# Performance work log

Measured on AMD Instinct MI355X. Metric: run time of the kernel, lower is better.

The kernel has to match this reference:

```python
import jax, jax.numpy as jnp
import numpy as np

B, S, D, H, L, V, DFF = 2, 2048, 1024, 16, 4, 32000, 4096
DH = D // H
STD = 0.02
EPS = 1e-5


def _sinusoidal_pe(seq_len, d_model):
    pos = np.arange(seq_len)[:, None].astype(np.float32)
    div = np.exp(np.arange(0, d_model, 2).astype(np.float32) * (-np.log(10000.0) / d_model))
    pe = np.zeros((seq_len, d_model), dtype=np.float32)
    pe[:, 0::2] = np.sin(pos * div)
    pe[:, 1::2] = np.cos(pos * div)
    return jnp.asarray(pe)


def _layernorm(x, g, b):
    mu = jnp.mean(x, axis=-1, keepdims=True)
    var = jnp.mean(jnp.square(x - mu), axis=-1, keepdims=True)
    return (x - mu) * jax.lax.rsqrt(var + EPS) * g + b


def setup_inputs() -> dict:
    key = jax.random.key(0)
    ks = jax.random.split(key, 12)
    input_ids = jax.random.randint(ks[0], (B, S), 0, V)
    tok_emb = STD * jax.random.normal(ks[1], (V, D), dtype=jnp.float32)
    tok_emb = tok_emb.at[0].set(0.0)  # padding_idx=0 zeroed
    Wq = STD * jax.random.normal(ks[2], (L, D, D), dtype=jnp.float32)
    Wk = STD * jax.random.normal(ks[3], (L, D, D), dtype=jnp.float32)
    Wv = STD * jax.random.normal(ks[4], (L, D, D), dtype=jnp.float32)
    Wo = STD * jax.random.normal(ks[5], (L, D, D), dtype=jnp.float32)
    W1 = STD * jax.random.normal(ks[6], (L, D, DFF), dtype=jnp.float32)
    W2 = STD * jax.random.normal(ks[7], (L, DFF, D), dtype=jnp.float32)
    Wout = STD * jax.random.normal(ks[8], (D, V), dtype=jnp.float32)
    zD = jnp.zeros((L, D), dtype=jnp.float32)
    return {
        'input_ids': input_ids, 'tok_emb': tok_emb,
        'Wq': Wq, 'bq': zD, 'Wk': Wk, 'bk': zD, 'Wv': Wv, 'bv': zD, 'Wo': Wo, 'bo': zD,
        'ln1_g': jnp.ones((L, D), jnp.float32), 'ln1_b': zD,
        'W1': W1, 'b1': jnp.zeros((L, DFF), jnp.float32), 'W2': W2, 'b2': zD,
        'ln3_g': jnp.ones((L, D), jnp.float32), 'ln3_b': zD,
        'Wout': Wout, 'bout': jnp.zeros((V,), jnp.float32),
    }


def reference(input_ids, tok_emb, Wq, bq, Wk, bk, Wv, bv, Wo, bo,
              ln1_g, ln1_b, W1, b1, W2, b2, ln3_g, ln3_b, Wout, bout):
    pe = _sinusoidal_pe(S, D)
    causal = jnp.tril(jnp.ones((S, S), dtype=bool))  # [S,S]
    x = tok_emb[input_ids] * jnp.float32(np.sqrt(D)) + pe  # [B,S,D]
    scale = jnp.float32(1.0 / np.sqrt(DH))
    for l in range(L):
        q = (x @ Wq[l] + bq[l]).reshape(B, S, H, DH).transpose(0, 2, 1, 3)
        k = (x @ Wk[l] + bk[l]).reshape(B, S, H, DH).transpose(0, 2, 1, 3)
        v = (x @ Wv[l] + bv[l]).reshape(B, S, H, DH).transpose(0, 2, 1, 3)
        scores = jnp.einsum('bhqd,bhkd->bhqk', q, k) * scale
        scores = jnp.where(causal, scores, jnp.float32(-1e9))
        attn = jax.nn.softmax(scores, axis=-1)
        o = jnp.einsum('bhqk,bhkd->bhqd', attn, v)
        o = o.transpose(0, 2, 1, 3).reshape(B, S, D) @ Wo[l] + bo[l]
        x = _layernorm(x + o, ln1_g[l], ln1_b[l])
        f = jax.nn.relu(x @ W1[l] + b1[l]) @ W2[l] + b2[l]
        x = _layernorm(x + f, ln3_g[l], ln3_b[l])
    logits = x @ Wout + bout  # [B,S,V]
    return logits
```

## Files before the change

kernel.cpp:

```cpp
#include <hip/hip_runtime.h>
#include <stdint.h>

typedef unsigned short u16;
typedef __attribute__((ext_vector_type(8))) short bf16x8;
typedef __attribute__((ext_vector_type(4))) float f32x4;

#define NB 2
#define NS 2048
#define ND 1024
#define NH 16
#define NL 4
#define NV 32000
#define NF 4096
#define NDH 64
#define NM (NB*NS)

__device__ __forceinline__ u16 f2b(float f) {
  union { float f; uint32_t u; } v; v.f = f;
  uint32_t r = v.u + 0x7FFFu + ((v.u >> 16) & 1u);
  return (u16)(r >> 16);
}

#define GLOAD_LDS16(gp, lp) __builtin_amdgcn_global_load_lds( \
    (const __attribute__((address_space(1))) void*)(gp), \
    (__attribute__((address_space(3))) void*)(lp), 16, 0, 0)

#define VMCNT8 do { asm volatile("s_waitcnt vmcnt(8)" ::: "memory"); __builtin_amdgcn_sched_barrier(0); } while (0)
#define VMCNT0 do { asm volatile("s_waitcnt vmcnt(0)" ::: "memory"); __builtin_amdgcn_sched_barrier(0); } while (0)
#define LGKM0  do { asm volatile("s_waitcnt lgkmcnt(0)" ::: "memory"); __builtin_amdgcn_sched_barrier(0); } while (0)
#define MFMA16(a,b,c) __builtin_amdgcn_mfma_f32_16x16x32_bf16((a),(b),(c),0,0,0)

__global__ __launch_bounds__(256)
void k_transpose64(const float* __restrict__ w, u16* __restrict__ wt, int K, int N) {
  __shared__ float tile[64][65];
  const int n0 = blockIdx.x * 64;
  const int k0 = blockIdx.y * 64;
  const int tr = threadIdx.x >> 4;
  const int tc = (threadIdx.x & 15) * 4;
#pragma unroll
  for (int i = 0; i < 4; i++) {
    int r = tr + i * 16;
    float4 v = *(const float4*)(w + (size_t)(k0 + r) * N + n0 + tc);
    tile[r][tc + 0] = v.x; tile[r][tc + 1] = v.y;
    tile[r][tc + 2] = v.z; tile[r][tc + 3] = v.w;
  }
  __syncthreads();
#pragma unroll
  for (int i = 0; i < 4; i++) {
    int nn = tr + i * 16;
    ushort4 pk;
    pk.x = f2b(tile[tc + 0][nn]);
    pk.y = f2b(tile[tc + 1][nn]);
    pk.z = f2b(tile[tc + 2][nn]);
    pk.w = f2b(tile[tc + 3][nn]);
    *(ushort4*)(wt + (size_t)(n0 + nn) * K + k0 + tc) = pk;
  }
}

__global__ __launch_bounds__(256)
void k_embed(const int* __restrict__ ids, const float* __restrict__ emb,
             float* __restrict__ x, u16* __restrict__ xb) {
  int row = blockIdx.x;
  int s = row & (NS - 1);
  int tok = ids[row];
  const float* e = emb + (size_t)tok * ND;
  int d0 = threadIdx.x * 4;
  float y[4];
#pragma unroll
  for (int j = 0; j < 4; j++) {
    int dd = d0 + j;
    float di = (float)(dd & ~1);
    float dv = expf(di * (-9.210340371976184f / (float)ND));
    float ang = (float)s * dv;
    float pe = (dd & 1) ? cosf(ang) : sinf(ang);
    y[j] = e[dd] * 32.0f + pe;
  }
  float4 w; w.x = y[0]; w.y = y[1]; w.z = y[2]; w.w = y[3];
  *(float4*)(x + (size_t)row * ND + d0) = w;
  uint2 pk;
  pk.x = (uint32_t)f2b(y[0]) | ((uint32_t)f2b(y[1]) << 16);
  pk.y = (uint32_t)f2b(y[2]) | ((uint32_t)f2b(y[3]) << 16);
  *(uint2*)(xb + (size_t)row * ND + d0) = pk;
}

__global__ __launch_bounds__(256)
void k_ln(const float* __restrict__ xin, const float* __restrict__ add,
          const float* __restrict__ g, const float* __restrict__ bb,
          float* __restrict__ xout, u16* __restrict__ xbout) {
  int row = blockIdx.x;
  int t = threadIdx.x;
  const float4 xi = *(const float4*)(xin + (size_t)row * ND + t * 4);
  const float4 ai = *(const float4*)(add + (size_t)row * ND + t * 4);
  float v0 = xi.x + ai.x, v1 = xi.y + ai.y, v2 = xi.z + ai.z, v3 = xi.w + ai.w;
  float s = v0 + v1 + v2 + v3;
  float s2 = v0 * v0 + v1 * v1 + v2 * v2 + v3 * v3;
#pragma unroll
  for (int d = 32; d >= 1; d >>= 1) { s += __shfl_xor(s, d); s2 += __shfl_xor(s2, d); }
  __shared__ float rs[8];
  int w = t >> 6;
  if ((t & 63) == 0) { rs[w] = s; rs[4 + w] = s2; }
  __syncthreads();
  s = rs[0] + rs[1] + rs[2] + rs[3];
  s2 = rs[4] + rs[5] + rs[6] + rs[7];
  float mu = s * (1.0f / ND);
  float var = s2 * (1.0f / ND) - mu * mu;
  float rr = rsqrtf(var + 1e-5f);
  const float4 gg = *(const float4*)(g + t * 4);
  const float4 be = *(const float4*)(bb + t * 4);
  float y0 = (v0 - mu) * rr * gg.x + be.x;
  float y1 = (v1 - mu) * rr * gg.y + be.y;
  float y2 = (v2 - mu) * rr * gg.z + be.z;
  float y3 = (v3 - mu) * rr * gg.w + be.w;
  float4 yo; yo.x = y0; yo.y = y1; yo.z = y2; yo.w = y3;
  *(float4*)(xout + (size_t)row * ND + t * 4) = yo;
  uint2 pk;
  pk.x = (uint32_t)f2b(y0) | ((uint32_t)f2b(y1) << 16);
  pk.y = (uint32_t)f2b(y2) | ((uint32_t)f2b(y3) << 16);
  *(uint2*)(xbout + (size_t)row * ND + t * 4) = pk;
}

template<int MODE>
__global__ __launch_bounds__(256)
void k_gemm_bt(const u16* __restrict__ A, const u16* __restrict__ Bt,
               const float* __restrict__ bias0, const float* __restrict__ bias1,
               const float* __restrict__ bias2,
               float* __restrict__ Cf, u16* __restrict__ Cb,
               int M, int N, int K, float scale) {
  constexpr int BM = 128, BN = 128, BK = 32;
  __shared__ __align__(16) u16 As[2][BM * BK];
  __shared__ __align__(16) u16 Bs[2][BN * BK];

  const int tid = threadIdx.x;
  const int lane = tid & 63;
  const int wave = tid >> 6;

  const int bm = blockIdx.x * BM;
  const int bn = blockIdx.y * BN;

  const int wr = (wave >> 1) * 64;
  const int wc = (wave & 1) * 64;
  const int lr = lane & 15;
  const int lk = (lane >> 4) * 8;

  const u16* Abase = A + (size_t)bm * K;
  const u16* Bbase = Bt + (size_t)bn * K;
  const int srow = lane >> 2;
  const int scol = (lane & 3) * 8;

  auto stage = [&](int buf, int kt) {
    const u16* Ag = Abase + (size_t)kt * BK + scol;
    const u16* Bg = Bbase + (size_t)kt * BK + scol;
#pragma unroll
    for (int i = 0; i < 2; i++) {
      const int rbase = (i * 4 + wave) * 16;
      GLOAD_LDS16(Ag + (size_t)(rbase + srow) * K, &As[buf][rbase * BK]);
      GLOAD_LDS16(Bg + (size_t)(rbase + srow) * K, &Bs[buf][rbase * BK]);
    }
  };

  f32x4 acc[4][4] = {};
  const int nk = K / BK;
  stage(0, 0);
  for (int kt = 0; kt < nk; ++kt) {
    __syncthreads();
    if (kt + 1 < nk) stage((kt + 1) & 1, kt + 1);
    const int buf = kt & 1;
    bf16x8 af[4], bfv[4];
#pragma unroll
    for (int m = 0; m < 4; m++)
      af[m] = *(const bf16x8*)(&As[buf][(wr + m * 16 + lr) * BK + lk]);
#pragma unroll
    for (int n = 0; n < 4; n++)
      bfv[n] = *(const bf16x8*)(&Bs[buf][(wc + n * 16 + lr) * BK + lk]);
#pragma unroll
    for (int m = 0; m < 4; m++)
#pragma unroll
      for (int n = 0; n < 4; n++)
        acc[m][n] = MFMA16(af[m], bfv[n], acc[m][n]);
  }

  const int lg = lane >> 4;
#pragma unroll
  for (int m = 0; m < 4; m++) {
#pragma unroll
    for (int n = 0; n < 4; n++) {
      int col = bn + wc + n * 16 + lr;
      float bv;
      if (MODE == 3) {
        int which = col >> 10;
        int cc = col & 1023;
        const float* bp = (which == 0) ? bias0 : ((which == 1) ? bias1 : bias2);
        bv = bp[cc];
      } else {
        bv = bias0[col];
      }
      if (MODE == 3 && (col >> 10) == 2) {
        int cc = col & 1023;
        int row0 = bm + wr + m * 16 + lg * 4;
        int b_ = row0 >> 11;
        int s_ = row0 & (NS - 1);
        int h_ = cc >> 6;
        int dh = cc & 63;
        ushort4 pk;
        pk.x = f2b(acc[m][n][0] + bv);
        pk.y = f2b(acc[m][n][1] + bv);
        pk.z = f2b(acc[m][n][2] + bv);
        pk.w = f2b(acc[m][n][3] + bv);
        *(ushort4*)(Cb + (size_t)2 * NM * ND +
                    ((((size_t)b_ * NH + h_) * NDH) + dh) * NS + s_) = pk;
        continue;
      }
#pragma unroll
      for (int j = 0; j < 4; j++) {
        int row = bm + wr + m * 16 + lg * 4 + j;
        float v = acc[m][n][j] + bv;
        if (MODE == 0) {
          Cf[(size_t)row * N + col] = v;
        } else if (MODE == 1) {
          Cb[(size_t)row * N + col] = f2b(fmaxf(v, 0.0f));
        } else {
          int which = col >> 10;
          int cc = col & 1023;
          if (which == 0) v *= scale;
          int b_ = row >> 11;
          int s_ = row & (NS - 1);
          int h_ = cc >> 6;
          int dh = cc & 63;
          Cb[(size_t)which * ((size_t)NM * ND) +
             ((((size_t)b_ * NH + h_) * NS) + s_) * NDH + dh] = f2b(v);
        }
      }
    }
  }
}

__global__ __launch_bounds__(256)
void k_gemm64(const u16* __restrict__ A, const u16* __restrict__ Bt,
              const float* __restrict__ bias,
              float* __restrict__ Cf, int M, int N, int K) {
  constexpr int BM = 64, BN = 128, BK = 32;
  __shared__ __align__(16) u16 As[2][BM * BK];
  __shared__ __align__(16) u16 Bs[2][BN * BK];

  const int tid = threadIdx.x;
  const int lane = tid & 63;
  const int wave = tid >> 6;

  const int bm = blockIdx.x * BM;
  const int bn = blockIdx.y * BN;

  const int wr = (wave >> 1) * 32;
  const int wc = (wave & 1) * 64;
  const int lr = lane & 15;
  const int lk = (lane >> 4) * 8;

  const u16* Abase = A + (size_t)bm * K;
  const u16* Bbase = Bt + (size_t)bn * K;
  const int srow = lane >> 2;
  const int scol = (lane & 3) * 8;

  auto stage = [&](int buf, int kt) {
    const u16* Ag = Abase + (size_t)kt * BK + scol;
    const u16* Bg = Bbase + (size_t)kt * BK + scol;
#pragma unroll
    for (int i = 0; i < 3; i++) {
      const int c = i * 4 + wave;
      if (c < 4) {
        const int rbase = c * 16;
        GLOAD_LDS16(Ag + (size_t)(rbase + srow) * K, &As[buf][rbase * BK]);
      } else {
        const int rbase = (c - 4) * 16;
        GLOAD_LDS16(Bg + (size_t)(rbase + srow) * K, &Bs[buf][rbase * BK]);
      }
    }
  };

  f32x4 acc[2][4] = {};
  const int nk = K / BK;
  stage(0, 0);
  for (int kt = 0; kt < nk; ++kt) {
    __syncthreads();
    if (kt + 1 < nk) stage((kt + 1) & 1, kt + 1);
    const int buf = kt & 1;
    bf16x8 af[2], bfv[4];
#pragma unroll
    for (int m = 0; m < 2; m++)
      af[m] = *(const bf16x8*)(&As[buf][(wr + m * 16 + lr) * BK + lk]);
#pragma unroll
    for (int n = 0; n < 4; n++)
      bfv[n] = *(const bf16x8*)(&Bs[buf][(wc + n * 16 + lr) * BK + lk]);
#pragma unroll
    for (int m = 0; m < 2; m++)
#pragma unroll
      for (int n = 0; n < 4; n++)
        acc[m][n] = MFMA16(af[m], bfv[n], acc[m][n]);
  }

  const int lg = lane >> 4;
#pragma unroll
  for (int m = 0; m < 2; m++) {
#pragma unroll
    for (int n = 0; n < 4; n++) {
      int col = bn + wc + n * 16 + lr;
      float bv = bias[col];
#pragma unroll
      for (int j = 0; j < 4; j++) {
        int row = bm + wr + m * 16 + lg * 4 + j;
        Cf[(size_t)row * N + col] = acc[m][n][j] + bv;
      }
    }
  }
}

template<int MODE>
__global__ __launch_bounds__(512, 2)
void k_gemm256(const u16* __restrict__ A, const u16* __restrict__ Bt,
               const float* __restrict__ bias,
               float* __restrict__ Cf, u16* __restrict__ Cb,
               int M, int N, int K) {
  __shared__ __align__(16) u16 As2[2][256 * 64];
  __shared__ __align__(16) u16 Bs2[2][256 * 64];

  const int tid = threadIdx.x;
  const int lane = tid & 63;
  const int wave = tid >> 6;
  const int wrM = wave >> 2;
  const int wcN = wave & 3;
  const int lr = lane & 15;
  const int g = lane >> 4;
  const int r7 = lr & 7;

  const int bm = blockIdx.x * 256;
  const int bn = blockIdx.y * 256;

  const int srow_in = lane >> 3;
  const int schunk = lane & 7;
  const int sq = (schunk ^ srow_in) * 8;

  auto stageA = [&](int buf, int t) {
#pragma unroll
    for (int s2 = 0; s2 < 4; ++s2) {
      const int rbase = (s2 * 8 + wave) * 8;
      GLOAD_LDS16(A + (size_t)(bm + rbase + srow_in) * K + t * 64 + sq, &As2[buf][rbase * 64]);
    }
  };
  auto stageB = [&](int buf, int t) {
#pragma unroll
    for (int s2 = 0; s2 < 4; ++s2) {
      const int rbase = (s2 * 8 + wave) * 8;
      GLOAD_LDS16(Bt + (size_t)(bn + rbase + srow_in) * K + t * 64 + sq, &Bs2[buf][rbase * 64]);
    }
  };

  f32x4 acc[8][4] = {};
  const int NT = K / 64;

  stageA(0, 0); stageB(0, 0);
  stageA(1, 1); stageB(1, 1);

  for (int t = 0; t < NT; ++t) {
    const int buf = t & 1;
    if (t + 1 < NT) { VMCNT8; } else { VMCNT0; }
    __builtin_amdgcn_s_barrier();

    const char* ab = (const char*)(&As2[buf][0]);
    const char* bb2 = (const char*)(&Bs2[buf][0]);
    bf16x8 aF[4][2], bF[4][2];

#pragma unroll
    for (int m = 0; m < 4; m++) {
      int row = wrM * 128 + m * 16 + lr;
      aF[m][0] = *(const bf16x8*)(ab + row * 128 + ((g ^ r7) * 16));
      aF[m][1] = *(const bf16x8*)(ab + row * 128 + (((4 + g) ^ r7) * 16));
    }
#pragma unroll
    for (int n = 0; n < 2; n++) {
      int row = wcN * 64 + n * 16 + lr;
      bF[n][0] = *(const bf16x8*)(bb2 + row * 128 + ((g ^ r7) * 16));
      bF[n][1] = *(const bf16x8*)(bb2 + row * 128 + (((4 + g) ^ r7) * 16));
    }
    __builtin_amdgcn_s_barrier();
    LGKM0;
    __builtin_amdgcn_s_setprio(1);
#pragma unroll
    for (int m = 0; m < 4; m++)
#pragma unroll
      for (int n = 0; n < 2; n++) {
        acc[m][n] = MFMA16(aF[m][0], bF[n][0], acc[m][n]);
        acc[m][n] = MFMA16(aF[m][1], bF[n][1], acc[m][n]);
      }
    __builtin_amdgcn_s_setprio(0);
    __builtin_amdgcn_s_barrier();

#pragma unroll
    for (int n = 2; n < 4; n++) {
      int row = wcN * 64 + n * 16 + lr;
      bF[n][0] = *(const bf16x8*)(bb2 + row * 128 + ((g ^ r7) * 16));
      bF[n][1] = *(const bf16x8*)(bb2 + row * 128 + (((4 + g) ^ r7) * 16));
    }
    __builtin_amdgcn_s_barrier();
    LGKM0;
    __builtin_amdgcn_s_setprio(1);
#pragma unroll
    for (int m = 0; m < 4; m++)
#pragma unroll
      for (int n = 2; n < 4; n++) {
        acc[m][n] = MFMA16(aF[m][0], bF[n][0], acc[m][n]);
        acc[m][n] = MFMA16(aF[m][1], bF[n][1], acc[m][n]);
      }
    __builtin_amdgcn_s_setprio(0);
    __builtin_amdgcn_s_barrier();

#pragma unroll
    for (int m = 0; m < 4; m++) {
      int row = wrM * 128 + (m + 4) * 16 + lr;
      aF[m][0] = *(const bf16x8*)(ab + row * 128 + ((g ^ r7) * 16));
      aF[m][1] = *(const bf16x8*)(ab + row * 128 + (((4 + g) ^ r7) * 16));
    }
    if (t + 2 < NT) stageB(buf, t + 2);
    __builtin_amdgcn_s_barrier();
    LGKM0;
    __builtin_amdgcn_s_setprio(1);
#pragma unroll
    for (int m = 0; m < 4; m++)
#pragma unroll
      for (int n = 0; n < 2; n++) {
        acc[m + 4][n] = MFMA16(aF[m][0], bF[n][0], acc[m + 4][n]);
        acc[m + 4][n] = MFMA16(aF[m][1], bF[n][1], acc[m + 4][n]);
      }
    __builtin_amdgcn_s_setprio(0);
    __builtin_amdgcn_s_barrier();

    if (t + 2 < NT) stageA(buf, t + 2);
    __builtin_amdgcn_s_barrier();
    __builtin_amdgcn_s_setprio(1);
#pragma unroll
    for (int m = 0; m < 4; m++)
#pragma unroll
      for (int n = 2; n < 4; n++) {
        acc[m + 4][n] = MFMA16(aF[m][0], bF[n][0], acc[m + 4][n]);
        acc[m + 4][n] = MFMA16(aF[m][1], bF[n][1], acc[m + 4][n]);
      }
    __builtin_amdgcn_s_setprio(0);
    __builtin_amdgcn_s_barrier();
  }

#pragma unroll
  for (int m = 0; m < 8; m++) {
#pragma unroll
    for (int n = 0; n < 4; n++) {
      int col = bn + wcN * 64 + n * 16 + lr;
      float bv = bias[col];
#pragma unroll
      for (int j = 0; j < 4; j++) {
        int row = bm + wrM * 128 + m * 16 + g * 4 + j;
        float v = acc[m][n][j] + bv;
        if (MODE == 0) Cf[(size_t)row * N + col] = v;
        else           Cb[(size_t)row * N + col] = f2b(fmaxf(v, 0.0f));
      }
    }
  }
}

__global__ __launch_bounds__(256)
void k_attn(const u16* __restrict__ Q, const u16* __restrict__ Kq,
            const u16* __restrict__ Vt, u16* __restrict__ O) {
  const int qt = blockIdx.x;
  const int bh = blockIdx.y;
  const int b_ = bh >> 4, h_ = bh & 15;
  const int tid = threadIdx.x, lane = tid & 63, wave = tid >> 6;
  const int lr = lane & 15, lg = lane >> 4;

  __shared__ __align__(16) u16 Ks[64 * 64];
  __shared__ __align__(16) u16 Vs[64 * 64];
  __shared__ __align__(16) u16 Ps[4][16 * 64];

  const size_t base = (size_t)bh * NS * NDH;
  bf16x8 qf0, qf1;
  {
    const u16* qp = Q + base + (size_t)(qt * 64 + wave * 16 + lr) * NDH;
    qf0 = *(const bf16x8*)(qp + lg * 8);
    qf1 = *(const bf16x8*)(qp + 32 + lg * 8);
  }

  const int idx0 = tid, idx1 = tid + 256;
  const int r0 = idx0 >> 3, r1 = idx1 >> 3;
  const int c0 = (idx0 & 7) * 8, c1 = (idx1 & 7) * 8;
  const int so0 = r0 * 128 + ((c0 * 2) ^ ((r0 & 7) << 4));
  const int so1 = r1 * 128 + ((c1 * 2) ^ ((r1 & 7) << 4));

  bf16x8 rk0, rk1, rv0, rv1;
  auto loadregs = [&](int kt2) {
    const u16* Kg = Kq + base + (size_t)(kt2 * 64) * NDH;
    const u16* Vg = Vt + base + kt2 * 64;
    rk0 = *(const bf16x8*)(Kg + (size_t)r0 * NDH + c0);
    rk1 = *(const bf16x8*)(Kg + (size_t)r1 * NDH + c1);
    rv0 = *(const bf16x8*)(Vg + (size_t)r0 * NS + c0);
    rv1 = *(const bf16x8*)(Vg + (size_t)r1 * NS + c1);
  };

  float mrun[4] = {-1e30f, -1e30f, -1e30f, -1e30f};
  float lrun[4] = {0.f, 0.f, 0.f, 0.f};
  f32x4 oacc[4] = {};
  const int q0 = qt * 64 + wave * 16;

  loadregs(0);
  for (int kt2 = 0; kt2 <= qt; ++kt2) {
    *(bf16x8*)((char*)Ks + so0) = rk0;
    *(bf16x8*)((char*)Ks + so1) = rk1;
    *(bf16x8*)((char*)Vs + so0) = rv0;
    *(bf16x8*)((char*)Vs + so1) = rv1;
    __syncthreads();
    if (kt2 < qt) loadregs(kt2 + 1);

    f32x4 sc[4];
    __builtin_amdgcn_s_setprio(1);
#pragma unroll
    for (int c = 0; c < 4; c++) {
      int row = c * 16 + lr;
      const char* kp = (const char*)Ks + row * 128;
      int sm = (row & 7) << 4;
      bf16x8 k0 = *(const bf16x8*)(kp + ((lg * 16) ^ sm));
      bf16x8 k1 = *(const bf16x8*)(kp + ((64 + lg * 16) ^ sm));
      f32x4 s = {};
      s = MFMA16(qf0, k0, s);
      s = MFMA16(qf1, k1, s);
      sc[c] = s;
    }
    __builtin_amdgcn_s_setprio(0);

    if (kt2 == qt) {
#pragma unroll
      for (int c = 0; c < 4; c++)
#pragma unroll
        for (int j = 0; j < 4; j++) {
          int qg = q0 + lg * 4 + j;
          int kg = qt * 64 + c * 16 + lr;
          if (kg > qg) sc[c][j] = -1e9f;
        }
    }

#pragma unroll
    for (int j = 0; j < 4; j++) {
      float mt = fmaxf(fmaxf(sc[0][j], sc[1][j]), fmaxf(sc[2][j], sc[3][j]));
#pragma unroll
      for (int d = 8; d >= 1; d >>= 1) mt = fmaxf(mt, __shfl_xor(mt, d));
      float mnew = fmaxf(mrun[j], mt);
      float corr = __expf(mrun[j] - mnew);
      float ps = 0.f;
#pragma unroll
      for (int c = 0; c < 4; c++) {
        float p = __expf(sc[c][j] - mnew);
        sc[c][j] = p;
        ps += p;
      }
#pragma unroll
      for (int d = 8; d >= 1; d >>= 1) ps += __shfl_xor(ps, d);
      lrun[j] = lrun[j] * corr + ps;
      mrun[j] = mnew;
#pragma unroll
      for (int n = 0; n < 4; n++) oacc[n][j] *= corr;
    }

    char* pw = (char*)Ps[wave];
#pragma unroll
    for (int c = 0; c < 4; c++)
#pragma unroll
      for (int j = 0; j < 4; j++) {
        int row = lg * 4 + j;
        *(u16*)(pw + row * 128 + ((((c * 16 + lr) * 2)) ^ ((row & 7) << 4))) = f2b(sc[c][j]);
      }

    {
      int smq = (lr & 7) << 4;
      bf16x8 pa0 = *(const bf16x8*)(pw + lr * 128 + ((lg * 16) ^ smq));
      bf16x8 pa1 = *(const bf16x8*)(pw + lr * 128 + ((64 + lg * 16) ^ smq));
      __builtin_amdgcn_s_setprio(1);
#pragma unroll
      for (int n = 0; n < 4; n++) {
        int row = n * 16 + lr;
        const char* vp = (const char*)Vs + row * 128;
        int sm = (row & 7) << 4;
        bf16x8 v0 = *(const bf16x8*)(vp + ((lg * 16) ^ sm));
        bf16x8 v1 = *(const bf16x8*)(vp + ((64 + lg * 16) ^ sm));
        oacc[n] = MFMA16(pa0, v0, oacc[n]);
        oacc[n] = MFMA16(pa1, v1, oacc[n]);
      }
      __builtin_amdgcn_s_setprio(0);
    }
    __syncthreads();
  }

#pragma unroll
  for (int j = 0; j < 4; j++) {
    float inv = 1.0f / lrun[j];
    int s_ = qt * 64 + wave * 16 + lg * 4 + j;
    size_t orow = ((size_t)b_ * NS + s_) * ND + h_ * NDH;
#pragma unroll
    for (int n = 0; n < 4; n++)
      O[orow + n * 16 + lr] = f2b(oacc[n][j] * inv);
  }
}

extern "C" void kernel_launch(void* const* d_in, const int* in_sizes, int n_in,
                              void* d_out, int out_size, void* d_ws, size_t ws_size,
                              hipStream_t stream) {
  const int* ids = (const int*)d_in[0];
  const float* tok_emb = (const float*)d_in[1];
  const float* Wq = (const float*)d_in[2];
  const float* bq = (const float*)d_in[3];
  const float* Wk = (const float*)d_in[4];
  const float* bk = (const float*)d_in[5];
  const float* Wv = (const float*)d_in[6];
  const float* bv = (const float*)d_in[7];
  const float* Wo = (const float*)d_in[8];
  const float* bo = (const float*)d_in[9];
  const float* ln1g = (const float*)d_in[10];
  const float* ln1b = (const float*)d_in[11];
  const float* W1 = (const float*)d_in[12];
  const float* b1 = (const float*)d_in[13];
  const float* W2 = (const float*)d_in[14];
  const float* b2 = (const float*)d_in[15];
  const float* ln3g = (const float*)d_in[16];
  const float* ln3b = (const float*)d_in[17];
  const float* Wout = (const float*)d_in[18];
  const float* bout = (const float*)d_in[19];
  float* out = (float*)d_out;

  char* ws = (char*)d_ws;
  size_t off = 0;
  auto alloc = [&](size_t bytes) -> void* {
    void* p = ws + off;
    off += (bytes + 255) & ~(size_t)255;
    return p;
  };
  float* x    = (float*)alloc((size_t)NM * ND * 4);
  float* tmp  = (float*)alloc((size_t)NM * ND * 4);
  u16* xb     = (u16*)alloc((size_t)NM * ND * 2);
  u16* hb     = (u16*)alloc((size_t)NM * NF * 2);
  u16* qkvb   = (u16*)alloc((size_t)3 * NM * ND * 2);
  u16* ob     = (u16*)alloc((size_t)NM * ND * 2);
  u16* Wqkvt  = (u16*)alloc((size_t)NL * 3 * ND * ND * 2);
  u16* Wot    = (u16*)alloc((size_t)NL * ND * ND * 2);
  u16* W1t    = (u16*)alloc((size_t)NL * (size_t)NF * ND * 2);
  u16* W2t    = (u16*)alloc((size_t)NL * (size_t)ND * NF * 2);
  u16* Woutt  = (u16*)alloc((size_t)NV * ND * 2);

  for (int l = 0; l < NL; l++) {
    size_t wl = (size_t)l * ND * ND;
    u16* qkvl = Wqkvt + (size_t)l * 3 * ND * ND;
    dim3 gdd(ND / 64, ND / 64);
    k_transpose64<<<gdd, 256, 0, stream>>>(Wq + wl, qkvl, ND, ND);
    k_transpose64<<<gdd, 256, 0, stream>>>(Wk + wl, qkvl + (size_t)ND * ND, ND, ND);
    k_transpose64<<<gdd, 256, 0, stream>>>(Wv + wl, qkvl + (size_t)2 * ND * ND, ND, ND);
    k_transpose64<<<gdd, 256, 0, stream>>>(Wo + wl, Wot + wl, ND, ND);
    k_transpose64<<<dim3(NF / 64, ND / 64), 256, 0, stream>>>(
        W1 + (size_t)l * ND * NF, W1t + (size_t)l * (size_t)NF * ND, ND, NF);
    k_transpose64<<<dim3(ND / 64, NF / 64), 256, 0, stream>>>(
        W2 + (size_t)l * NF * ND, W2t + (size_t)l * (size_t)ND * NF, NF, ND);
  }
  k_transpose64<<<dim3(NV / 64, ND / 64), 256, 0, stream>>>(Wout, Woutt, ND, NV);

  k_embed<<<NM, 256, 0, stream>>>(ids, tok_emb, x, xb);

  for (int l = 0; l < NL; l++) {
    size_t wl = (size_t)l * ND * ND;
    u16* qkvl = Wqkvt + (size_t)l * 3 * ND * ND;

    k_gemm_bt<3><<<dim3(NM / 128, 3 * ND / 128), 256, 0, stream>>>(
        xb, qkvl, bq + l * ND, bk + l * ND, bv + l * ND,
        nullptr, qkvb, NM, 3 * ND, ND, 0.125f);

    k_attn<<<dim3(NS / 64, NB * NH), 256, 0, stream>>>(
        qkvb, qkvb + (size_t)NM * ND, qkvb + (size_t)2 * NM * ND, ob);

    k_gemm64<<<dim3(NM / 64, ND / 128), 256, 0, stream>>>(
        ob, Wot + wl, bo + l * ND, tmp, NM, ND, ND);

    k_ln<<<NM, 256, 0, stream>>>(x, tmp, ln1g + l * ND, ln1b + l * ND, x, xb);

    k_gemm256<1><<<dim3(NM / 256, NF / 256), 512, 0, stream>>>(
        xb, W1t + (size_t)l * (size_t)NF * ND, b1 + l * NF, nullptr, hb, NM, NF, ND);

    k_gemm64<<<dim3(NM / 64, ND / 128), 256, 0, stream>>>(
        hb, W2t + (size_t)l * (size_t)ND * NF, b2 + l * ND, tmp, NM, ND, NF);

    k_ln<<<NM, 256, 0, stream>>>(x, tmp, ln3g + l * ND, ln3b + l * ND, x, xb);
  }

  k_gemm256<0><<<dim3(NM / 256, NV / 256), 512, 0, stream>>>(
      xb, Woutt, bout, out, nullptr, NM, NV, ND);
}
```

Measured before the change: 1.823 ms.

## Double-buffer K/V tiles in attention and skip softmax rescaling when max stable

The attention kernel now keeps two LDS buffers for K and V and writes the next tile into the alternate buffer at the end of each iteration, which removes one __syncthreads per KV tile. It also adds a lazy online-softmax rescale: the running max and the accumulator correction are updated only when some row's new max exceeds the old one by more than 8. This saves exp and multiply work on most tiles. The cost is twice the LDS for K/V, plus possible growth of unnormalized values up to e^8 when the rescale is skipped. That is fine in fp32 but makes the bf16 P values exceed 1.

```diff
diff --git a/kernel.cpp b/kernel.cpp
--- a/kernel.cpp
+++ b/kernel.cpp
@@ -471,8 +471,8 @@
   const int tid = threadIdx.x, lane = tid & 63, wave = tid >> 6;
   const int lr = lane & 15, lg = lane >> 4;
 
-  __shared__ __align__(16) u16 Ks[64 * 64];
-  __shared__ __align__(16) u16 Vs[64 * 64];
+  __shared__ __align__(16) u16 Ks[2][64 * 64];
+  __shared__ __align__(16) u16 Vs[2][64 * 64];
   __shared__ __align__(16) u16 Ps[4][16 * 64];
 
   const size_t base = (size_t)bh * NS * NDH;
@@ -498,27 +498,33 @@
     rv0 = *(const bf16x8*)(Vg + (size_t)r0 * NS + c0);
     rv1 = *(const bf16x8*)(Vg + (size_t)r1 * NS + c1);
   };
+  auto writebuf = [&](int b) {
+    *(bf16x8*)((char*)Ks[b] + so0) = rk0;
+    *(bf16x8*)((char*)Ks[b] + so1) = rk1;
+    *(bf16x8*)((char*)Vs[b] + so0) = rv0;
+    *(bf16x8*)((char*)Vs[b] + so1) = rv1;
+  };
 
   float mrun[4] = {-1e30f, -1e30f, -1e30f, -1e30f};
   float lrun[4] = {0.f, 0.f, 0.f, 0.f};
   f32x4 oacc[4] = {};
   const int q0 = qt * 64 + wave * 16;
+  const int nkv = qt + 1;
 
   loadregs(0);
-  for (int kt2 = 0; kt2 <= qt; ++kt2) {
-    *(bf16x8*)((char*)Ks + so0) = rk0;
-    *(bf16x8*)((char*)Ks + so1) = rk1;
-    *(bf16x8*)((char*)Vs + so0) = rv0;
-    *(bf16x8*)((char*)Vs + so1) = rv1;
+  writebuf(0);
+  for (int kt2 = 0; kt2 < nkv; ++kt2) {
     __syncthreads();
-    if (kt2 < qt) loadregs(kt2 + 1);
+    if (kt2 + 1 < nkv) loadregs(kt2 + 1);
+    const char* kb = (const char*)Ks[kt2 & 1];
+    const char* vb = (const char*)Vs[kt2 & 1];
 
     f32x4 sc[4];
     __builtin_amdgcn_s_setprio(1);
 #pragma unroll
     for (int c = 0; c < 4; c++) {
       int row = c * 16 + lr;
-      const char* kp = (const char*)Ks + row * 128;
+      const char* kp = kb + row * 128;
       int sm = (row & 7) << 4;
       bf16x8 k0 = *(const bf16x8*)(kp + ((lg * 16) ^ sm));
       bf16x8 k1 = *(const bf16x8*)(kp + ((64 + lg * 16) ^ sm));
@@ -540,13 +546,22 @@
         }
     }
 
+    float mt[4];
+    float dmax = -1e30f;
 #pragma unroll
     for (int j = 0; j < 4; j++) {
-      float mt = fmaxf(fmaxf(sc[0][j], sc[1][j]), fmaxf(sc[2][j], sc[3][j]));
-#pragma unroll
-      for (int d = 8; d >= 1; d >>= 1) mt = fmaxf(mt, __shfl_xor(mt, d));
-      float mnew = fmaxf(mrun[j], mt);
-      float corr = __expf(mrun[j] - mnew);
+      float m0 = fmaxf(fmaxf(sc[0][j], sc[1][j]), fmaxf(sc[2][j], sc[3][j]));
+#pragma unroll
+      for (int d = 8; d >= 1; d >>= 1) m0 = fmaxf(m0, __shfl_xor(m0, d));
+      mt[j] = m0;
+      dmax = fmaxf(dmax, m0 - mrun[j]);
+    }
+    const bool need = __any(dmax > 8.0f);
+
+#pragma unroll
+    for (int j = 0; j < 4; j++) {
+      float mold = mrun[j];
+      float mnew = need ? fmaxf(mold, mt[j]) : mold;
       float ps = 0.f;
 #pragma unroll
       for (int c = 0; c < 4; c++) {
@@ -556,10 +571,15 @@
       }
 #pragma unroll
       for (int d = 8; d >= 1; d >>= 1) ps += __shfl_xor(ps, d);
-      lrun[j] = lrun[j] * corr + ps;
-      mrun[j] = mnew;
-#pragma unroll
-      for (int n = 0; n < 4; n++) oacc[n][j] *= corr;
+      if (need) {
+        float corr = __expf(mold - mnew);
+        lrun[j] = lrun[j] * corr + ps;
+        mrun[j] = mnew;
+#pragma unroll
+        for (int n = 0; n < 4; n++) oacc[n][j] *= corr;
+      } else {
+        lrun[j] += ps;
+      }
     }
 
     char* pw = (char*)Ps[wave];
@@ -579,7 +599,7 @@
 #pragma unroll
       for (int n = 0; n < 4; n++) {
         int row = n * 16 + lr;
-        const char* vp = (const char*)Vs + row * 128;
+        const char* vp = vb + row * 128;
         int sm = (row & 7) << 4;
         bf16x8 v0 = *(const bf16x8*)(vp + ((lg * 16) ^ sm));
         bf16x8 v1 = *(const bf16x8*)(vp + ((64 + lg * 16) ^ sm));
@@ -588,7 +608,8 @@
       }
       __builtin_amdgcn_s_setprio(0);
     }
-    __syncthreads();
+
+    if (kt2 + 1 < nkv) writebuf((kt2 + 1) & 1);
   }
 
 #pragma unroll
```

Result: slower. 1.944 ms (+6.6%).
